# Optimization experiments

Hardware: AMD Instinct MI355X
Metric: run time of the kernel (lower is better)

Reference implementation:

```python
import jax, jax.numpy as jnp
import numpy as np

B, S, H = 4, 2048, 1024
E, K, INTER = 16, 2, 512
ALPHA, LIMIT = 1.702, 7.0


def setup_inputs() -> dict:
    key = jax.random.key(0)
    ks = jax.random.split(key, 6)
    return {
        "hidden_states": jax.random.normal(ks[0], (B, S, H), jnp.float32),
        "router_weight": jax.random.normal(ks[1], (H, E), jnp.float32) * 0.02,
        "gate_up_proj": jax.random.normal(ks[2], (E, H, 2 * INTER), jnp.float32) * 0.02,
        "gate_up_proj_bias": jax.random.normal(ks[3], (E, 2 * INTER), jnp.float32) * 0.02,
        "down_proj": jax.random.normal(ks[4], (E, INTER, H), jnp.float32) * 0.02,
        "down_proj_bias": jax.random.normal(ks[5], (E, H), jnp.float32) * 0.02,
    }


def reference(hidden_states, router_weight, gate_up_proj, gate_up_proj_bias,
              down_proj, down_proj_bias):
    b, s, h = hidden_states.shape
    x = hidden_states.reshape(-1, h)  # [T, H]
    # Router: linear logits -> top-k -> softmax over selected -> sparse scores [T, E]
    logits = x @ router_weight                      # [T, E]
    topk_w, topk_i = jax.lax.top_k(logits, K)       # [T, K]
    topk_w = jax.nn.softmax(topk_w, axis=-1)
    one_hot = (topk_i[..., None] == jnp.arange(E)[None, None, :]).astype(topk_w.dtype)
    scores = jnp.einsum('tk,tke->te', topk_w, one_hot)  # [T, E]
    # Fused gate+up projection per expert (num_devices=1 => dispatch/combine identity)
    gu = jnp.einsum('th,ehf->tef', x, gate_up_proj) + gate_up_proj_bias  # [T, E, 2I]
    gate = gu[..., ::2]   # interleaved layout
    up = gu[..., 1::2]
    # gpt_oss activation: clamp + scaled sigmoid glu
    gate = jnp.minimum(gate, LIMIT)
    up = jnp.clip(up, -LIMIT, LIMIT)
    glu = gate * jax.nn.sigmoid(gate * ALPHA)
    act = (up + 1.0) * glu                          # [T, E, I]
    # Down projection + score-weighted combine
    out = jnp.einsum('tei,eih,te->th', act, down_proj, scores)
    out = out + jnp.einsum('te,eh->th', scores, down_proj_bias)
    return out.reshape(b, s, h)
```

## Files before the change

### kernel.cpp

```cpp
#include <hip/hip_runtime.h>
#include <hip/hip_bf16.h>
#include <math.h>

#define TOK   8192
#define HDIM  1024
#define NE    16
#define NI    512
#define F2    1024
#define CAP   8192
#define CAP2  2048
#define ALPHA 1.702f
#define LIMIT 7.0f

typedef __attribute__((ext_vector_type(8))) short short8;
typedef __attribute__((ext_vector_type(4))) short short4v;
typedef __attribute__((ext_vector_type(4))) float f32x4;

static __device__ __forceinline__ unsigned short f2bf(float f) {
    unsigned int u = __float_as_uint(f);
    u += 0x7FFFu + ((u >> 16) & 1u);
    return (unsigned short)(u >> 16);
}
static __device__ __forceinline__ float bf2f(unsigned short u) {
    return __uint_as_float((unsigned int)u << 16);
}

#define GLD_LDS16(g, l) __builtin_amdgcn_global_load_lds(                     \
    (const __attribute__((address_space(1))) void*)(g),                       \
    (__attribute__((address_space(3))) void*)(l), 16, 0, 0)

__global__ __launch_bounds__(64) void router_partial_kernel(
    const float* __restrict__ x, const float* __restrict__ rw,
    double* __restrict__ part, unsigned short* __restrict__ xbf)
{
    int bx = blockIdx.x;
    int tile = bx >> 2, ksl = bx & 3;
    int t0 = tile * 16;
    int hbase = ksl * 256;

    __shared__ __align__(16) float sx[16][68];
    __shared__ __align__(16) float srw[64][16];

    int lane = threadIdx.x;
    int tt = lane & 15, eg = lane >> 4;

    double acc[4] = {0.0, 0.0, 0.0, 0.0};

    for (int hc = 0; hc < 4; ++hc) {
        int h0 = hbase + hc * 64;
        __syncthreads();
#pragma unroll
        for (int j = 0; j < 4; ++j) {
            int fidx = j * 64 + lane;
            int t = fidx >> 4, c4 = (fidx & 15) * 4;
            float4 v = *(const float4*)(x + (size_t)(t0 + t) * HDIM + h0 + c4);
            *(float4*)&sx[t][c4] = v;
            short4v s;
            s[0] = (short)f2bf(v.x); s[1] = (short)f2bf(v.y);
            s[2] = (short)f2bf(v.z); s[3] = (short)f2bf(v.w);
            *(short4v*)(xbf + (size_t)(t0 + t) * HDIM + h0 + c4) = s;
        }
#pragma unroll
        for (int j = 0; j < 4; ++j) {
            int ridx = j * 64 + lane;
            int h = ridx >> 2, e4 = (ridx & 3) * 4;
            float4 v = *(const float4*)(rw + (size_t)(h0 + h) * NE + e4);
            *(float4*)&srw[h][e4] = v;
        }
        __syncthreads();
#pragma unroll 8
        for (int j = 0; j < 64; ++j) {
            float xv = sx[tt][j];
            float4 wv = *(const float4*)&srw[j][eg * 4];
            double xd = (double)xv;
            acc[0] += xd * (double)wv.x;
            acc[1] += xd * (double)wv.y;
            acc[2] += xd * (double)wv.z;
            acc[3] += xd * (double)wv.w;
        }
    }
#pragma unroll
    for (int q = 0; q < 4; ++q)
        part[(size_t)(ksl * NE + eg * 4 + q) * TOK + t0 + tt] = acc[q];
}

__global__ __launch_bounds__(256) void router_combine_kernel(
    const double* __restrict__ part,
    int* __restrict__ counts, int* __restrict__ toks, float* __restrict__ wgts,
    unsigned short* __restrict__ inv)
{
    __shared__ int lhist[NE];
    __shared__ int lbase[NE];
    int tid = threadIdx.x;
    int t = blockIdx.x * 256 + tid;
    if (tid < NE) lhist[tid] = 0;
    __syncthreads();

    double acc[NE];
#pragma unroll
    for (int e = 0; e < NE; ++e)
        acc[e] = part[(size_t)(0 * NE + e) * TOK + t]
               + part[(size_t)(1 * NE + e) * TOK + t]
               + part[(size_t)(2 * NE + e) * TOK + t]
               + part[(size_t)(3 * NE + e) * TOK + t];

    int i0 = 0; double v0 = acc[0];
#pragma unroll
    for (int e = 1; e < NE; ++e) if (acc[e] > v0) { v0 = acc[e]; i0 = e; }
    int i1 = -1; double v1 = -1e300;
#pragma unroll
    for (int e = 0; e < NE; ++e) if (e != i0 && acc[e] > v1) { v1 = acc[e]; i1 = e; }
    double e1 = exp(v1 - v0);
    float w0 = (float)(1.0 / (1.0 + e1));
    float w1 = (float)(e1 / (1.0 + e1));

    int r0 = atomicAdd(&lhist[i0], 1);
    int r1 = atomicAdd(&lhist[i1], 1);
    __syncthreads();
    if (tid < NE) lbase[tid] = atomicAdd(&counts[tid], lhist[tid]);
    __syncthreads();
    int p0 = lbase[i0] + r0; if (p0 > 2047) p0 = 2047;
    int p1 = lbase[i1] + r1; if (p1 > 2047) p1 = 2047;
    toks[i0 * CAP + p0] = t; wgts[i0 * CAP + p0] = w0;
    toks[i1 * CAP + p1] = t; wgts[i1 * CAP + p1] = w1;
    inv[2 * t]     = (unsigned short)((i0 << 11) | p0);
    inv[2 * t + 1] = (unsigned short)((i1 << 11) | p1);
}

__global__ __launch_bounds__(256) void transpose_kernel(
    const float* __restrict__ in, unsigned short* __restrict__ out, int R, int C, int perm)
{
    int e = blockIdx.z;
    const float* pin = in + (size_t)e * R * C;
    unsigned short* pout = out + (size_t)e * R * C;
    __shared__ float t2[64][65];
    int c0 = blockIdx.x * 64, r0 = blockIdx.y * 64;
    int tid = threadIdx.x;
#pragma unroll
    for (int j = 0; j < 4; ++j) {
        int idx4 = j * 256 + tid;
        int r = idx4 >> 4, c4 = (idx4 & 15) * 4;
        float4 v = *(const float4*)(pin + (size_t)(r0 + r) * C + c0 + c4);
        t2[c4 + 0][r] = v.x;
        t2[c4 + 1][r] = v.y;
        t2[c4 + 2][r] = v.z;
        t2[c4 + 3][r] = v.w;
    }
    __syncthreads();
#pragma unroll
    for (int j = 0; j < 2; ++j) {
        int idx = j * 256 + tid;
        int n = idx >> 3, k0 = (idx & 7) * 8;
        short8 v;
#pragma unroll
        for (int q = 0; q < 8; ++q) v[q] = (short)f2bf(t2[n][k0 + q]);
        int c = c0 + n;
        int orow;
        if (perm) {
            int tile = c >> 7, ct = c & 127;
            int fl = ct >> 1, h = ct & 1;
            orow = (tile << 7) | ((fl >> 4) << 5) | (h << 4) | (fl & 15);
        } else {
            orow = c;
        }
        *(short8*)(pout + (size_t)orow * R + r0 + k0) = v;
    }
}

#define KLOOP_BODY(NT, KOFF)                                                          \
    int c0 = 0;                                                                       \
    for (int kb = 0; kb < (NT); ++kb) {                                               \
        if (kb + 2 < (NT)) {                                                          \
            int cpre = c0 + 2; if (cpre >= 3) cpre -= 3;                              \
            _Pragma("unroll")                                                         \
            for (int i = 0; i < 2; ++i) {                                             \
                GLD_LDS16(gaA[i] + (kb + 2) * (KOFF), &As[cpre][w * 32 + i * 16][0]); \
                GLD_LDS16(gaB[i] + (kb + 2) * (KOFF), &Bs[cpre][w * 32 + i * 16][0]); \
            }                                                                         \
            asm volatile("s_waitcnt vmcnt(8)" ::: "memory");                          \
        } else if (kb + 1 < (NT)) {                                                   \
            asm volatile("s_waitcnt vmcnt(4)" ::: "memory");                          \
        } else {                                                                      \
            asm volatile("s_waitcnt vmcnt(0)" ::: "memory");                          \
        }                                                                             \
        __builtin_amdgcn_sched_barrier(0);                                            \
        __builtin_amdgcn_s_barrier();                                                 \
        __builtin_amdgcn_sched_barrier(0);                                            \
        short8 af[4], bfr[4];                                                         \
        _Pragma("unroll")                                                             \
        for (int m = 0; m < 4; ++m) af[m] = *(const short8*)&As[c0][wr * 64 + m * 16 + lr][slt]; \
        _Pragma("unroll")                                                             \
        for (int n = 0; n < 4; ++n) bfr[n] = *(const short8*)&Bs[c0][wc * 64 + n * 16 + lr][slt]; \
        _Pragma("unroll")                                                             \
        for (int m = 0; m < 4; ++m)                                                   \
            _Pragma("unroll")                                                         \
            for (int n = 0; n < 4; ++n)                                               \
                acc[m][n] = __builtin_amdgcn_mfma_f32_16x16x32_bf16(af[m], bfr[n], acc[m][n], 0, 0, 0); \
        asm volatile("s_waitcnt lgkmcnt(0)" ::: "memory");                            \
        __builtin_amdgcn_sched_barrier(0);                                            \
        __builtin_amdgcn_s_barrier();                                                 \
        __builtin_amdgcn_sched_barrier(0);                                            \
        c0 = (c0 + 1 == 3) ? 0 : c0 + 1;                                              \
    }

#define KLOOP_PROLOGUE(KOFF)                                                          \
    _Pragma("unroll")                                                                 \
    for (int i = 0; i < 2; ++i) {                                                     \
        GLD_LDS16(gaA[i], &As[0][w * 32 + i * 16][0]);                                \
        GLD_LDS16(gaB[i], &Bs[0][w * 32 + i * 16][0]);                                \
    }                                                                                 \
    _Pragma("unroll")                                                                 \
    for (int i = 0; i < 2; ++i) {                                                     \
        GLD_LDS16(gaA[i] + (KOFF), &As[1][w * 32 + i * 16][0]);                       \
        GLD_LDS16(gaB[i] + (KOFF), &Bs[1][w * 32 + i * 16][0]);                       \
    }

__global__ __launch_bounds__(256) void gemm1_kernel(
    const unsigned short* __restrict__ xb, const unsigned short* __restrict__ gupT,
    const float* __restrict__ gub,
    const int* __restrict__ counts, const int* __restrict__ toks,
    unsigned short* __restrict__ act, const unsigned short* __restrict__ zp)
{
    int b = blockIdx.x;
    int e = b & 15;
    int j = b >> 4;
    int nt = j & 7;
    int mt = j >> 3;
    int cnt = counts[e];
    int row0 = mt * 128;
    if (row0 >= cnt) return;
    int n0 = nt * 128;

    __shared__ __align__(16) unsigned short As[3][128][32];
    __shared__ __align__(16) unsigned short Bs[3][128][32];
    __shared__ int rtok[128];

    int tid = threadIdx.x;
    int lane = tid & 63;
    int w = tid >> 6;
    int wr = w >> 1, wc = w & 1;
    int lr = lane & 15, lg = lane >> 4;

    if (tid < 128) {
        int p = row0 + tid;
        rtok[tid] = (p < cnt) ? toks[e * CAP + p] : -1;
    }
    __syncthreads();

    int srow = lane >> 2;
    int scol = (((lane & 3) ^ ((lane >> 3) & 3)) * 8);
    int slt = (lg ^ ((lr >> 1) & 3)) * 8;

    const unsigned short* gaA[2];
    const unsigned short* gaB[2];
    const unsigned short* gupE = gupT + (size_t)e * HDIM * F2;
#pragma unroll
    for (int i = 0; i < 2; ++i) {
        int arow = w * 32 + i * 16 + srow;
        int tk = rtok[arow];
        gaA[i] = (tk >= 0) ? (xb + (size_t)tk * HDIM + scol) : (zp + scol);
        int brow = n0 + w * 32 + i * 16 + srow;
        gaB[i] = gupE + (size_t)brow * HDIM + scol;
    }

    f32x4 acc[4][4];
#pragma unroll
    for (int m = 0; m < 4; ++m)
#pragma unroll
        for (int n = 0; n < 4; ++n) acc[m][n] = (f32x4){0.f, 0.f, 0.f, 0.f};

    KLOOP_PROLOGUE(32)
    KLOOP_BODY(HDIM / 32, 32)

    unsigned short* actE = act + (size_t)e * CAP2 * NI;
    int fbase = nt * 64 + wc * 32;
#pragma unroll
    for (int q = 0; q < 2; ++q) {
        int f = fbase + q * 16 + lr;
        float bg = gub[e * F2 + 2 * f];
        float bu = gub[e * F2 + 2 * f + 1];
#pragma unroll
        for (int m = 0; m < 4; ++m) {
#pragma unroll
            for (int r = 0; r < 4; ++r) {
                float gate = acc[m][2 * q][r] + bg;
                float up   = acc[m][2 * q + 1][r] + bu;
                gate = fminf(gate, LIMIT);
                up   = fminf(fmaxf(up, -LIMIT), LIMIT);
                float glu = gate / (1.0f + __expf(-ALPHA * gate));
                float av  = (up + 1.0f) * glu;
                int row = row0 + wr * 64 + m * 16 + lg * 4 + r;
                actE[(size_t)row * NI + f] = f2bf(av);
            }
        }
    }
}

__global__ __launch_bounds__(256) void gemm2_y_kernel(
    const unsigned short* __restrict__ act, const unsigned short* __restrict__ dwnT,
    const float* __restrict__ dwb,
    const int* __restrict__ counts, const float* __restrict__ wgts,
    unsigned short* __restrict__ y)
{
    int b = blockIdx.x;
    int e = b & 15;
    int j = b >> 4;
    int nt = j & 7;
    int mt = j >> 3;
    int cnt = counts[e];
    int row0 = mt * 128;
    if (row0 >= cnt) return;
    int n0 = nt * 128;

    int base_e = 0;
#pragma unroll
    for (int q = 0; q < NE; ++q) base_e += (q < e) ? counts[q] : 0;

    __shared__ __align__(16) unsigned short As[3][128][32];
    __shared__ __align__(16) unsigned short Bs[3][128][32];
    __shared__ float rwgt[128];

    int tid = threadIdx.x;
    int lane = tid & 63;
    int w = tid >> 6;
    int wr = w >> 1, wc = w & 1;
    int lr = lane & 15, lg = lane >> 4;

    if (tid < 128) {
        int p = row0 + tid;
        rwgt[tid] = (p < cnt) ? wgts[e * CAP + p] : 0.0f;
    }
    __syncthreads();

    int srow = lane >> 2;
    int scol = (((lane & 3) ^ ((lane >> 3) & 3)) * 8);
    int slt = (lg ^ ((lr >> 1) & 3)) * 8;

    const unsigned short* gaA[2];
    const unsigned short* gaB[2];
    const unsigned short* actE = act + (size_t)e * CAP2 * NI;
    const unsigned short* dwnE = dwnT + (size_t)e * HDIM * NI;
#pragma unroll
    for (int i = 0; i < 2; ++i) {
        int arow = row0 + w * 32 + i * 16 + srow;
        gaA[i] = actE + (size_t)arow * NI + scol;
        int brow = n0 + w * 32 + i * 16 + srow;
        gaB[i] = dwnE + (size_t)brow * NI + scol;
    }

    f32x4 acc[4][4];
#pragma unroll
    for (int m = 0; m < 4; ++m)
#pragma unroll
        for (int n = 0; n < 4; ++n) acc[m][n] = (f32x4){0.f, 0.f, 0.f, 0.f};

    KLOOP_PROLOGUE(32)
    KLOOP_BODY(NI / 32, 32)

    unsigned short* yB = y + (size_t)(base_e + row0) * HDIM;
#pragma unroll
    for (int n = 0; n < 4; ++n) {
        int hc = n0 + wc * 64 + n * 16 + lr;
        float db = dwb[e * HDIM + hc];
#pragma unroll
        for (int m = 0; m < 4; ++m) {
#pragma unroll
            for (int r = 0; r < 4; ++r) {
                int rl = wr * 64 + m * 16 + lg * 4 + r;
                if (row0 + rl < cnt)
                    yB[(size_t)rl * HDIM + hc] = f2bf(rwgt[rl] * (acc[m][n][r] + db));
            }
        }
    }
}

__global__ __launch_bounds__(256) void out_combine_kernel(
    const unsigned short* __restrict__ y, const unsigned short* __restrict__ inv,
    const int* __restrict__ counts, float* __restrict__ out)
{
    __shared__ int sbase[NE];
    int tid = threadIdx.x;
    int t = blockIdx.x;
    if (tid == 0) {
        int s = 0;
#pragma unroll
        for (int e = 0; e < NE; ++e) { sbase[e] = s; s += counts[e]; }
    }
    __syncthreads();
    unsigned short v0 = inv[2 * t], v1 = inv[2 * t + 1];
    int s0 = sbase[v0 >> 11] + (v0 & 2047);
    int s1 = sbase[v1 >> 11] + (v1 & 2047);
    short4v a = *(const short4v*)(y + (size_t)s0 * HDIM + tid * 4);
    short4v c = *(const short4v*)(y + (size_t)s1 * HDIM + tid * 4);
    float4 o;
    o.x = bf2f((unsigned short)a[0]) + bf2f((unsigned short)c[0]);
    o.y = bf2f((unsigned short)a[1]) + bf2f((unsigned short)c[1]);
    o.z = bf2f((unsigned short)a[2]) + bf2f((unsigned short)c[2]);
    o.w = bf2f((unsigned short)a[3]) + bf2f((unsigned short)c[3]);
    *(float4*)(out + (size_t)t * HDIM + tid * 4) = o;
}

__global__ __launch_bounds__(256) void router_kernel(
    const float* __restrict__ x, const float* __restrict__ rw,
    int* __restrict__ counts, int* __restrict__ toks, float* __restrict__ wgts)
{
    int gwave = (int)((blockIdx.x * 256 + threadIdx.x) >> 6);
    int lane = threadIdx.x & 63;
    if (gwave >= TOK) return;
    const float* xr = x + (size_t)gwave * HDIM;
    double acc[NE];
#pragma unroll
    for (int e = 0; e < NE; ++e) acc[e] = 0.0;
    for (int i = 0; i < HDIM / 64; ++i) {
        int h = i * 64 + lane;
        double xv = (double)xr[h];
        const float* r = rw + (size_t)h * NE;
#pragma unroll
        for (int e = 0; e < NE; ++e) acc[e] += xv * (double)r[e];
    }
#pragma unroll
    for (int e = 0; e < NE; ++e) {
        double v = acc[e];
#pragma unroll
        for (int off = 32; off > 0; off >>= 1) v += __shfl_xor(v, off);
        acc[e] = v;
    }
    if (lane == 0) {
        int i0 = 0; double v0 = acc[0];
#pragma unroll
        for (int e = 1; e < NE; ++e) if (acc[e] > v0) { v0 = acc[e]; i0 = e; }
        int i1 = -1; double v1 = -1e300;
#pragma unroll
        for (int e = 0; e < NE; ++e) if (e != i0 && acc[e] > v1) { v1 = acc[e]; i1 = e; }
        double e1 = exp(v1 - v0);
        float w0 = (float)(1.0 / (1.0 + e1));
        float w1 = (float)(e1 / (1.0 + e1));
        int p0 = atomicAdd(&counts[i0], 1);
        toks[i0 * CAP + p0] = gwave; wgts[i0 * CAP + p0] = w0;
        int p1 = atomicAdd(&counts[i1], 1);
        toks[i1 * CAP + p1] = gwave; wgts[i1 * CAP + p1] = w1;
    }
}

__global__ __launch_bounds__(256) void moe_kernel(
    const float* __restrict__ x,
    const float* __restrict__ gup, const float* __restrict__ gub,
    const float* __restrict__ dwn, const float* __restrict__ dwb,
    const int* __restrict__ counts, const int* __restrict__ toks,
    const float* __restrict__ wgts, float* __restrict__ out)
{
    int e = blockIdx.y;
    int cnt = counts[e];
    int row0 = blockIdx.x * 64;
    if (row0 >= cnt) return;

    __shared__ __align__(16) unsigned short sA[64][40];
    __shared__ __align__(16) unsigned short sB[64][40];
    __shared__ __align__(16) unsigned short sAct[64][520];
    __shared__ int   rtok[64];
    __shared__ float rwgt[64];

    int tid = threadIdx.x;
    if (tid < 64) {
        int idx = row0 + tid;
        bool v = idx < cnt;
        rtok[tid] = v ? toks[e * CAP + idx] : -1;
        rwgt[tid] = v ? wgts[e * CAP + idx] : 0.0f;
    }
    __syncthreads();

    int lane = tid & 63;
    int w = tid >> 6;
    int wr = w >> 1, wc = w & 1;
    int lr = lane & 15, lg = lane >> 4;
    int ar = tid >> 2, ac0 = (tid & 3) * 8;
    int bk = tid >> 3, bf0 = (tid & 7) * 8;
    const float* gupE = gup + (size_t)e * HDIM * F2;

    for (int nb = 0; nb < F2 / 64; ++nb) {
        f32x4 acc[2][2];
#pragma unroll
        for (int mi = 0; mi < 2; ++mi)
#pragma unroll
            for (int ni = 0; ni < 2; ++ni) acc[mi][ni] = (f32x4){0.f, 0.f, 0.f, 0.f};
        for (int kb = 0; kb < HDIM / 32; ++kb) {
            __syncthreads();
            {
                int tk = rtok[ar];
                short8 vv = {0,0,0,0,0,0,0,0};
                if (tk >= 0) {
                    const float* p = x + (size_t)tk * HDIM + kb * 32 + ac0;
                    float4 u0 = *(const float4*)(p); float4 u1 = *(const float4*)(p + 4);
                    vv[0]=(short)f2bf(u0.x); vv[1]=(short)f2bf(u0.y); vv[2]=(short)f2bf(u0.z); vv[3]=(short)f2bf(u0.w);
                    vv[4]=(short)f2bf(u1.x); vv[5]=(short)f2bf(u1.y); vv[6]=(short)f2bf(u1.z); vv[7]=(short)f2bf(u1.w);
                }
                *(short8*)&sA[ar][ac0] = vv;
            }
            {
                const float* p = gupE + (size_t)(kb * 32 + bk) * F2 + nb * 64 + bf0;
                float4 u0 = *(const float4*)(p); float4 u1 = *(const float4*)(p + 4);
                sB[bf0+0][bk]=f2bf(u0.x); sB[bf0+1][bk]=f2bf(u0.y); sB[bf0+2][bk]=f2bf(u0.z); sB[bf0+3][bk]=f2bf(u0.w);
                sB[bf0+4][bk]=f2bf(u1.x); sB[bf0+5][bk]=f2bf(u1.y); sB[bf0+6][bk]=f2bf(u1.z); sB[bf0+7][bk]=f2bf(u1.w);
            }
            __syncthreads();
            short8 a0 = *(const short8*)&sA[wr*32+lr][lg*8];
            short8 a1 = *(const short8*)&sA[wr*32+16+lr][lg*8];
            short8 b0 = *(const short8*)&sB[wc*32+lr][lg*8];
            short8 b1 = *(const short8*)&sB[wc*32+16+lr][lg*8];
            acc[0][0] = __builtin_amdgcn_mfma_f32_16x16x32_bf16(a0,b0,acc[0][0],0,0,0);
            acc[0][1] = __builtin_amdgcn_mfma_f32_16x16x32_bf16(a0,b1,acc[0][1],0,0,0);
            acc[1][0] = __builtin_amdgcn_mfma_f32_16x16x32_bf16(a1,b0,acc[1][0],0,0,0);
            acc[1][1] = __builtin_amdgcn_mfma_f32_16x16x32_bf16(a1,b1,acc[1][1],0,0,0);
        }
#pragma unroll
        for (int ni = 0; ni < 2; ++ni) {
            int fc = nb * 64 + wc * 32 + ni * 16 + lr;
            float bias = gub[e * F2 + fc];
#pragma unroll
            for (int mi = 0; mi < 2; ++mi)
#pragma unroll
                for (int r = 0; r < 4; ++r) {
                    float gu = acc[mi][ni][r] + bias;
                    float other = __shfl_xor(gu, 1);
                    float gate = (lr & 1) ? other : gu;
                    float up   = (lr & 1) ? gu : other;
                    gate = fminf(gate, LIMIT);
                    up = fminf(fmaxf(up, -LIMIT), LIMIT);
                    float glu = gate / (1.0f + __expf(-ALPHA * gate));
                    float av = (up + 1.0f) * glu;
                    if (!(lr & 1)) sAct[wr*32+mi*16+lg*4+r][fc >> 1] = f2bf(av);
                }
        }
    }
    __syncthreads();

    const float* dwnE = dwn + (size_t)e * NI * HDIM;
    int tks[2][4]; float wvs[2][4];
#pragma unroll
    for (int mi = 0; mi < 2; ++mi)
#pragma unroll
        for (int r = 0; r < 4; ++r) {
            int row = wr*32 + mi*16 + lg*4 + r;
            tks[mi][r] = rtok[row]; wvs[mi][r] = rwgt[row];
        }
    for (int nb = 0; nb < HDIM / 64; ++nb) {
        f32x4 acc[2][2];
#pragma unroll
        for (int mi = 0; mi < 2; ++mi)
#pragma unroll
            for (int ni = 0; ni < 2; ++ni) acc[mi][ni] = (f32x4){0.f,0.f,0.f,0.f};
        for (int kb = 0; kb < NI / 32; ++kb) {
            __syncthreads();
            {
                const float* p = dwnE + (size_t)(kb*32 + bk) * HDIM + nb*64 + bf0;
                float4 u0 = *(const float4*)(p); float4 u1 = *(const float4*)(p + 4);
                sB[bf0+0][bk]=f2bf(u0.x); sB[bf0+1][bk]=f2bf(u0.y); sB[bf0+2][bk]=f2bf(u0.z); sB[bf0+3][bk]=f2bf(u0.w);
                sB[bf0+4][bk]=f2bf(u1.x); sB[bf0+5][bk]=f2bf(u1.y); sB[bf0+6][bk]=f2bf(u1.z); sB[bf0+7][bk]=f2bf(u1.w);
            }
            __syncthreads();
            short8 a0 = *(const short8*)&sAct[wr*32+lr][kb*32+lg*8];
            short8 a1 = *(const short8*)&sAct[wr*32+16+lr][kb*32+lg*8];
            short8 b0 = *(const short8*)&sB[wc*32+lr][lg*8];
            short8 b1 = *(const short8*)&sB[wc*32+16+lr][lg*8];
            acc[0][0] = __builtin_amdgcn_mfma_f32_16x16x32_bf16(a0,b0,acc[0][0],0,0,0);
            acc[0][1] = __builtin_amdgcn_mfma_f32_16x16x32_bf16(a0,b1,acc[0][1],0,0,0);
            acc[1][0] = __builtin_amdgcn_mfma_f32_16x16x32_bf16(a1,b0,acc[1][0],0,0,0);
            acc[1][1] = __builtin_amdgcn_mfma_f32_16x16x32_bf16(a1,b1,acc[1][1],0,0,0);
        }
#pragma unroll
        for (int ni = 0; ni < 2; ++ni) {
            int hc = nb*64 + wc*32 + ni*16 + lr;
            float db = dwb[e * HDIM + hc];
#pragma unroll
            for (int mi = 0; mi < 2; ++mi)
#pragma unroll
                for (int r = 0; r < 4; ++r) {
                    int tk = tks[mi][r];
                    if (tk >= 0)
                        atomicAdd(out + (size_t)tk * HDIM + hc, wvs[mi][r] * (acc[mi][ni][r] + db));
                }
        }
    }
}

extern "C" void kernel_launch(void* const* d_in, const int* in_sizes, int n_in,
                              void* d_out, int out_size, void* d_ws, size_t ws_size,
                              hipStream_t stream) {
    const float* x   = (const float*)d_in[0];
    const float* rw  = (const float*)d_in[1];
    const float* gup = (const float*)d_in[2];
    const float* gub = (const float*)d_in[3];
    const float* dwn = (const float*)d_in[4];
    const float* dwb = (const float*)d_in[5];
    float* out = (float*)d_out;

    const size_t OFF_COUNTS = 0;
    const size_t OFF_ZP     = 256;
    const size_t OFF_INV    = 4352;
    const size_t OFF_TOKS   = OFF_INV  + (size_t)TOK * 2 * 2;
    const size_t OFF_WGTS   = OFF_TOKS + (size_t)NE * CAP * 4;
    const size_t OFF_DWNT   = OFF_WGTS + (size_t)NE * CAP * 4;
    const size_t OFF_ACT    = OFF_DWNT + (size_t)NE * NI * HDIM * 2;
    const size_t OFF_XBF    = OFF_ACT  + (size_t)NE * CAP2 * NI * 2;
    const size_t OFF_GUPT   = OFF_XBF  + (size_t)TOK * HDIM * 2;
    const size_t REQ_B      = OFF_GUPT + (size_t)NE * HDIM * F2 * 2;
    const size_t OFF_Y      = OFF_XBF;
    const size_t REQ_A      = OFF_Y + (size_t)2 * TOK * HDIM * 2;

    if (ws_size >= REQ_B) {
        int*            counts = (int*)((char*)d_ws + OFF_COUNTS);
        unsigned short* zp     = (unsigned short*)((char*)d_ws + OFF_ZP);
        unsigned short* inv    = (unsigned short*)((char*)d_ws + OFF_INV);
        int*            toks   = (int*)((char*)d_ws + OFF_TOKS);
        float*          wgts   = (float*)((char*)d_ws + OFF_WGTS);
        unsigned short* dwnT   = (unsigned short*)((char*)d_ws + OFF_DWNT);
        unsigned short* act    = (unsigned short*)((char*)d_ws + OFF_ACT);
        double*         part   = (double*)((char*)d_ws + OFF_ACT);
        unsigned short* xbf    = (unsigned short*)((char*)d_ws + OFF_XBF);
        unsigned short* gupT   = (unsigned short*)((char*)d_ws + OFF_GUPT);
        unsigned short* y      = (unsigned short*)((char*)d_ws + OFF_Y);

        hipMemsetAsync(d_ws, 0, 4352, stream);

        dim3 tg1(F2 / 64, HDIM / 64, NE);
        transpose_kernel<<<tg1, 256, 0, stream>>>(gup, gupT, HDIM, F2, 1);
        dim3 tg2(HDIM / 64, NI / 64, NE);
        transpose_kernel<<<tg2, 256, 0, stream>>>(dwn, dwnT, NI, HDIM, 0);

        router_partial_kernel<<<(TOK / 16) * 4, 64, 0, stream>>>(x, rw, part, xbf);
        router_combine_kernel<<<TOK / 256, 256, 0, stream>>>(part, counts, toks, wgts, inv);

        int g1 = (CAP2 / 128) * (F2 / 128) * NE;
        gemm1_kernel<<<g1, 256, 0, stream>>>(xbf, gupT, gub, counts, toks, act, zp);
        int g2 = (CAP2 / 128) * (HDIM / 128) * NE;

        if (ws_size >= REQ_A) {
            gemm2_y_kernel<<<g2, 256, 0, stream>>>(act, dwnT, dwb, counts, wgts, y);
            out_combine_kernel<<<TOK, 256, 0, stream>>>(y, inv, counts, out);
        } else {
            hipMemsetAsync(d_out, 0, (size_t)out_size * sizeof(float), stream);
            out_combine_kernel<<<TOK, 256, 0, stream>>>(y, inv, counts, out);
        }
    } else {
        int*   counts = (int*)d_ws;
        int*   toks   = (int*)((char*)d_ws + 64);
        float* wgts   = (float*)((char*)d_ws + 64 + (size_t)NE * CAP * sizeof(int));
        hipMemsetAsync(d_ws, 0, 64, stream);
        hipMemsetAsync(d_out, 0, (size_t)out_size * sizeof(float), stream);
        router_kernel<<<TOK / 4, 256, 0, stream>>>(x, rw, counts, toks, wgts);
        dim3 gm(TOK / 64, NE);
        moe_kernel<<<gm, 256, 0, stream>>>(x, gup, gub, dwn, dwb, counts, toks, wgts, out);
    }
}
```

Measured before the change: 168.3 us.

## Enlarge GEMM tiles to 256x128 with 512-thread blocks

Both expert GEMM kernels move from 128x128 tiles with 256 threads to 256-row by 128-column tiles with 8 waves, so each B tile staged in LDS is reused across twice as many rows. Per-thread staging changes to two A loads and one B load, with adjusted vmcnt waits. The goal is less weight-tile traffic and fewer blocks. In exchange the block needs more LDS, occupancy may drop, and larger row tiles waste more work on partly filled expert tails.

Result: slower. 179.0 us (+6.3%).

```diff
diff --git a/kernel.cpp b/kernel.cpp
--- a/kernel.cpp
+++ b/kernel.cpp
@@ -167,19 +167,20 @@
     }
 }
 
-#define KLOOP_BODY(NT, KOFF)                                                          \
-    int c0 = 0;                                                                       \
+#define STAGE_TILE(buf, kidx)                                                         \
+    GLD_LDS16(gaA[0] + (size_t)(kidx) * 32, &As[buf][w * 32][0]);                     \
+    GLD_LDS16(gaA[1] + (size_t)(kidx) * 32, &As[buf][w * 32 + 16][0]);                \
+    GLD_LDS16(gaB0   + (size_t)(kidx) * 32, &Bs[buf][w * 16][0]);
+
+#define KLOOP_BODY(NT)                                                                \
+    int cb = 0;                                                                       \
     for (int kb = 0; kb < (NT); ++kb) {                                               \
         if (kb + 2 < (NT)) {                                                          \
-            int cpre = c0 + 2; if (cpre >= 3) cpre -= 3;                              \
-            _Pragma("unroll")                                                         \
-            for (int i = 0; i < 2; ++i) {                                             \
-                GLD_LDS16(gaA[i] + (kb + 2) * (KOFF), &As[cpre][w * 32 + i * 16][0]); \
-                GLD_LDS16(gaB[i] + (kb + 2) * (KOFF), &Bs[cpre][w * 32 + i * 16][0]); \
-            }                                                                         \
-            asm volatile("s_waitcnt vmcnt(8)" ::: "memory");                          \
+            int cpre = cb + 2; if (cpre >= 3) cpre -= 3;                              \
+            STAGE_TILE(cpre, kb + 2)                                                  \
+            asm volatile("s_waitcnt vmcnt(6)" ::: "memory");                          \
         } else if (kb + 1 < (NT)) {                                                   \
-            asm volatile("s_waitcnt vmcnt(4)" ::: "memory");                          \
+            asm volatile("s_waitcnt vmcnt(3)" ::: "memory");                          \
         } else {                                                                      \
             asm volatile("s_waitcnt vmcnt(0)" ::: "memory");                          \
         }                                                                             \
@@ -188,9 +189,9 @@
         __builtin_amdgcn_sched_barrier(0);                                            \
         short8 af[4], bfr[4];                                                         \
         _Pragma("unroll")                                                             \
-        for (int m = 0; m < 4; ++m) af[m] = *(const short8*)&As[c0][wr * 64 + m * 16 + lr][slt]; \
+        for (int m = 0; m < 4; ++m) af[m] = *(const short8*)&As[cb][wr * 64 + m * 16 + lr][slt]; \
         _Pragma("unroll")                                                             \
-        for (int n = 0; n < 4; ++n) bfr[n] = *(const short8*)&Bs[c0][wc * 64 + n * 16 + lr][slt]; \
+        for (int n = 0; n < 4; ++n) bfr[n] = *(const short8*)&Bs[cb][wc * 64 + n * 16 + lr][slt]; \
         _Pragma("unroll")                                                             \
         for (int m = 0; m < 4; ++m)                                                   \
             _Pragma("unroll")                                                         \
@@ -200,22 +201,10 @@
         __builtin_amdgcn_sched_barrier(0);                                            \
         __builtin_amdgcn_s_barrier();                                                 \
         __builtin_amdgcn_sched_barrier(0);                                            \
-        c0 = (c0 + 1 == 3) ? 0 : c0 + 1;                                              \
-    }
-
-#define KLOOP_PROLOGUE(KOFF)                                                          \
-    _Pragma("unroll")                                                                 \
-    for (int i = 0; i < 2; ++i) {                                                     \
-        GLD_LDS16(gaA[i], &As[0][w * 32 + i * 16][0]);                                \
-        GLD_LDS16(gaB[i], &Bs[0][w * 32 + i * 16][0]);                                \
-    }                                                                                 \
-    _Pragma("unroll")                                                                 \
-    for (int i = 0; i < 2; ++i) {                                                     \
-        GLD_LDS16(gaA[i] + (KOFF), &As[1][w * 32 + i * 16][0]);                       \
-        GLD_LDS16(gaB[i] + (KOFF), &Bs[1][w * 32 + i * 16][0]);                       \
-    }
-
-__global__ __launch_bounds__(256) void gemm1_kernel(
+        cb = (cb + 1 == 3) ? 0 : cb + 1;                                              \
+    }
+
+__global__ __launch_bounds__(512) void gemm1_kernel(
     const unsigned short* __restrict__ xb, const unsigned short* __restrict__ gupT,
     const float* __restrict__ gub,
     const int* __restrict__ counts, const int* __restrict__ toks,
@@ -227,13 +216,13 @@
     int nt = j & 7;
     int mt = j >> 3;
     int cnt = counts[e];
-    int row0 = mt * 128;
+    int row0 = mt * 256;
     if (row0 >= cnt) return;
     int n0 = nt * 128;
 
-    __shared__ __align__(16) unsigned short As[3][128][32];
+    __shared__ __align__(16) unsigned short As[3][256][32];
     __shared__ __align__(16) unsigned short Bs[3][128][32];
-    __shared__ int rtok[128];
+    __shared__ int rtok[256];
 
     int tid = threadIdx.x;
     int lane = tid & 63;
@@ -241,7 +230,7 @@
     int wr = w >> 1, wc = w & 1;
     int lr = lane & 15, lg = lane >> 4;
 
-    if (tid < 128) {
+    if (tid < 256) {
         int p = row0 + tid;
         rtok[tid] = (p < cnt) ? toks[e * CAP + p] : -1;
     }
@@ -249,18 +238,20 @@
 
     int srow = lane >> 2;
     int scol = (((lane & 3) ^ ((lane >> 3) & 3)) * 8);
-    int slt = (lg ^ ((lr >> 1) & 3)) * 8;
+    int slt  = (lg ^ ((lr >> 1) & 3)) * 8;
 
     const unsigned short* gaA[2];
-    const unsigned short* gaB[2];
+    const unsigned short* gaB0;
     const unsigned short* gupE = gupT + (size_t)e * HDIM * F2;
 #pragma unroll
     for (int i = 0; i < 2; ++i) {
         int arow = w * 32 + i * 16 + srow;
         int tk = rtok[arow];
         gaA[i] = (tk >= 0) ? (xb + (size_t)tk * HDIM + scol) : (zp + scol);
-        int brow = n0 + w * 32 + i * 16 + srow;
-        gaB[i] = gupE + (size_t)brow * HDIM + scol;
+    }
+    {
+        int brow = n0 + w * 16 + srow;
+        gaB0 = gupE + (size_t)brow * HDIM + scol;
     }
 
     f32x4 acc[4][4];
@@ -269,8 +260,9 @@
 #pragma unroll
         for (int n = 0; n < 4; ++n) acc[m][n] = (f32x4){0.f, 0.f, 0.f, 0.f};
 
-    KLOOP_PROLOGUE(32)
-    KLOOP_BODY(HDIM / 32, 32)
+    STAGE_TILE(0, 0)
+    STAGE_TILE(1, 1)
+    KLOOP_BODY(HDIM / 32)
 
     unsigned short* actE = act + (size_t)e * CAP2 * NI;
     int fbase = nt * 64 + wc * 32;
@@ -296,7 +288,7 @@
     }
 }
 
-__global__ __launch_bounds__(256) void gemm2_y_kernel(
+__global__ __launch_bounds__(512) void gemm2_y_kernel(
     const unsigned short* __restrict__ act, const unsigned short* __restrict__ dwnT,
     const float* __restrict__ dwb,
     const int* __restrict__ counts, const float* __restrict__ wgts,
@@ -308,7 +300,7 @@
     int nt = j & 7;
     int mt = j >> 3;
     int cnt = counts[e];
-    int row0 = mt * 128;
+    int row0 = mt * 256;
     if (row0 >= cnt) return;
     int n0 = nt * 128;
 
@@ -316,9 +308,9 @@
 #pragma unroll
     for (int q = 0; q < NE; ++q) base_e += (q < e) ? counts[q] : 0;
 
-    __shared__ __align__(16) unsigned short As[3][128][32];
+    __shared__ __align__(16) unsigned short As[3][256][32];
     __shared__ __align__(16) unsigned short Bs[3][128][32];
-    __shared__ float rwgt[128];
+    __shared__ float rwgt[256];
 
     int tid = threadIdx.x;
     int lane = tid & 63;
@@ -326,7 +318,7 @@
     int wr = w >> 1, wc = w & 1;
     int lr = lane & 15, lg = lane >> 4;
 
-    if (tid < 128) {
+    if (tid < 256) {
         int p = row0 + tid;
         rwgt[tid] = (p < cnt) ? wgts[e * CAP + p] : 0.0f;
     }
@@ -334,18 +326,20 @@
 
     int srow = lane >> 2;
     int scol = (((lane & 3) ^ ((lane >> 3) & 3)) * 8);
-    int slt = (lg ^ ((lr >> 1) & 3)) * 8;
+    int slt  = (lg ^ ((lr >> 1) & 3)) * 8;
 
     const unsigned short* gaA[2];
-    const unsigned short* gaB[2];
+    const unsigned short* gaB0;
     const unsigned short* actE = act + (size_t)e * CAP2 * NI;
     const unsigned short* dwnE = dwnT + (size_t)e * HDIM * NI;
 #pragma unroll
     for (int i = 0; i < 2; ++i) {
         int arow = row0 + w * 32 + i * 16 + srow;
         gaA[i] = actE + (size_t)arow * NI + scol;
-        int brow = n0 + w * 32 + i * 16 + srow;
-        gaB[i] = dwnE + (size_t)brow * NI + scol;
+    }
+    {
+        int brow = n0 + w * 16 + srow;
+        gaB0 = dwnE + (size_t)brow * NI + scol;
     }
 
     f32x4 acc[4][4];
@@ -354,8 +348,9 @@
 #pragma unroll
         for (int n = 0; n < 4; ++n) acc[m][n] = (f32x4){0.f, 0.f, 0.f, 0.f};
 
-    KLOOP_PROLOGUE(32)
-    KLOOP_BODY(NI / 32, 32)
+    STAGE_TILE(0, 0)
+    STAGE_TILE(1, 1)
+    KLOOP_BODY(NI / 32)
 
     unsigned short* yB = y + (size_t)(base_e + row0) * HDIM;
 #pragma unroll
@@ -630,12 +625,12 @@
         router_partial_kernel<<<(TOK / 16) * 4, 64, 0, stream>>>(x, rw, part, xbf);
         router_combine_kernel<<<TOK / 256, 256, 0, stream>>>(part, counts, toks, wgts, inv);
 
-        int g1 = (CAP2 / 128) * (F2 / 128) * NE;
-        gemm1_kernel<<<g1, 256, 0, stream>>>(xbf, gupT, gub, counts, toks, act, zp);
-        int g2 = (CAP2 / 128) * (HDIM / 128) * NE;
+        int g1 = NE * (F2 / 128) * (CAP2 / 256);
+        gemm1_kernel<<<g1, 512, 0, stream>>>(xbf, gupT, gub, counts, toks, act, zp);
+        int g2 = NE * (HDIM / 128) * (CAP2 / 256);
 
         if (ws_size >= REQ_A) {
-            gemm2_y_kernel<<<g2, 256, 0, stream>>>(act, dwnT, dwb, counts, wgts, y);
+            gemm2_y_kernel<<<g2, 512, 0, stream>>>(act, dwnT, dwb, counts, wgts, y);
             out_combine_kernel<<<TOK, 256, 0, stream>>>(y, inv, counts, out);
         } else {
             hipMemsetAsync(d_out, 0, (size_t)out_size * sizeof(float), stream);
```
